# Performance work log

Hardware: AMD Instinct MI355X
Metric: run time of the kernel (lower is better)

## Reference

```python
import jax, jax.numpy as jnp
import numpy as np

B, D_IN, D_LAT, K = 8192, 768, 12288, 64


def setup_inputs() -> dict:
    key = jax.random.key(0)
    k1, k2, k3 = jax.random.split(key, 3)
    x = jax.random.normal(k1, (B, D_IN), dtype=jnp.float32)
    # Kaiming-uniform-ish init scale (matches nn.Linear default magnitude)
    W_enc = jax.random.normal(k2, (D_IN, D_LAT), dtype=jnp.float32) * (1.0 / np.sqrt(D_IN))
    b_enc = jnp.zeros((D_LAT,), dtype=jnp.float32)
    W_dec = jax.random.normal(k3, (D_LAT, D_IN), dtype=jnp.float32) * (1.0 / np.sqrt(D_LAT))
    b_dec = jnp.zeros((D_IN,), dtype=jnp.float32)
    return {"x": x, "W_enc": W_enc, "b_enc": b_enc, "W_dec": W_dec, "b_dec": b_dec, "k_top": K}


def topk_activation(h, k):
    # keep top-k values per row, zero the rest (equivalent to zeros_like + scatter_)
    if k >= h.shape[1]:
        return h
    vals, idx = jax.lax.top_k(h, k)                  # [B, k]
    rows = jnp.arange(h.shape[0])[:, None]           # [B, 1]
    return jnp.zeros_like(h).at[rows, idx].set(vals)


def reference(x, W_enc, b_enc, W_dec, b_dec, k_top):
    h = x @ W_enc + b_enc                            # [B, D_LAT]
    z = topk_activation(h, k_top)                    # sparse latent [B, D_LAT]
    recon = z @ W_dec + b_dec                        # [B, D_IN]
    return recon, z
```

## Files before the change

kernel.cpp:

```cpp
#include <hip/hip_runtime.h>
#include <stdint.h>

#define BROWS 8192
#define DIN   768
#define DLAT  12288
#define KTOP  64

#define LO_SCALE 4096.0f
#define LO_INV   (1.0f / 4096.0f)


typedef _Float16 half8 __attribute__((ext_vector_type(8)));
typedef __attribute__((ext_vector_type(4))) float float4v;

typedef __attribute__((address_space(3))) void lds_void_t;
typedef __attribute__((address_space(1))) void glob_void_t;

__device__ __forceinline__ unsigned short f2h_bits(float f) {
  _Float16 h = (_Float16)f;
  return __builtin_bit_cast(unsigned short, h);
}
__device__ __forceinline__ float h_bits_to_f(unsigned short b) {
  return (float)__builtin_bit_cast(_Float16, b);
}

__global__ __launch_bounds__(256) void k_cvt_split(const float* __restrict__ in,
                                                   unsigned short* __restrict__ hi,
                                                   unsigned short* __restrict__ lo,
                                                   int n4) {
  int i = blockIdx.x * 256 + threadIdx.x;
  if (i >= n4) return;
  float4 v = ((const float4*)in)[i];
  ushort4 h, l;
  h.x = f2h_bits(v.x); l.x = f2h_bits((v.x - h_bits_to_f(h.x)) * LO_SCALE);
  h.y = f2h_bits(v.y); l.y = f2h_bits((v.y - h_bits_to_f(h.y)) * LO_SCALE);
  h.z = f2h_bits(v.z); l.z = f2h_bits((v.z - h_bits_to_f(h.z)) * LO_SCALE);
  h.w = f2h_bits(v.w); l.w = f2h_bits((v.w - h_bits_to_f(h.w)) * LO_SCALE);
  ((ushort4*)hi)[i] = h;
  ((ushort4*)lo)[i] = l;
}

__global__ __launch_bounds__(256) void k_transpose_split(const float* __restrict__ W,
                                                         unsigned short* __restrict__ Wth,
                                                         unsigned short* __restrict__ Wtl) {
  __shared__ float s[32][33];
  const int n0 = blockIdx.x * 32;
  const int k0 = blockIdx.y * 32;
  const int tx = threadIdx.x, ty = threadIdx.y;
#pragma unroll
  for (int i = 0; i < 4; i++)
    s[ty + 8 * i][tx] = W[(size_t)(k0 + ty + 8 * i) * DLAT + n0 + tx];
  __syncthreads();
#pragma unroll
  for (int i = 0; i < 4; i++) {
    int nl = ty + 8 * i;
    float v = s[tx][nl];
    unsigned short h = f2h_bits(v);
    unsigned short l = f2h_bits((v - h_bits_to_f(h)) * LO_SCALE);
    size_t o = (size_t)(n0 + nl) * DIN + k0 + tx;
    Wth[o] = h;
    Wtl[o] = l;
  }
}

#define GBM 256
#define GBN 128
#define GBK 32

#define MFMA12(MI, AH, AL)                                                                   \
  do {                                                                                       \
    _Pragma("unroll") for (int ni = 0; ni < 4; ni++) {                                       \
      acc1[MI][ni] = __builtin_amdgcn_mfma_f32_16x16x32_f16(AH, bh[ni], acc1[MI][ni], 0, 0, 0); \
      acc2[MI][ni] = __builtin_amdgcn_mfma_f32_16x16x32_f16(AL, bh[ni], acc2[MI][ni], 0, 0, 0); \
      acc2[MI][ni] = __builtin_amdgcn_mfma_f32_16x16x32_f16(AH, bl[ni], acc2[MI][ni], 0, 0, 0); \
    }                                                                                        \
  } while (0)

#define STAGE1(R)                                                                            \
  __builtin_amdgcn_global_load_lds((glob_void_t*)(src[R] + kk2),                             \
                                   (lds_void_t*)(sb + loff[R]), 16, 0, 0)

__global__ __launch_bounds__(512, 2) void k_enc_gemm(const unsigned short* __restrict__ Xh,
                                                     const unsigned short* __restrict__ Xl,
                                                     const unsigned short* __restrict__ Wth,
                                                     const unsigned short* __restrict__ Wtl,
                                                     const float* __restrict__ b_enc,
                                                     float* __restrict__ H) {
  __shared__ unsigned short lds[3][24576];

  const int tid  = threadIdx.x;
  const int lane = tid & 63;
  const int wave = tid >> 6;
  const int wm   = wave >> 1;
  const int wn   = wave & 1;

  const int wg = (blockIdx.x & 7) * 384 + (blockIdx.x >> 3);
  const int tm = wg / 96;
  const int tn = wg - tm * 96;
  const int m_blk = tm * GBM;
  const int n_blk = tn * GBN;

  const int qlog = (lane & 3) ^ ((lane >> 3) & 3);
  const unsigned short* src[6];
  int loff[6];
#pragma unroll
  for (int r = 0; r < 6; r++) {
    const int c = wave * 6 + r;
    const unsigned short* base;
    int grow;
    if (c < 16)      { base = Xh;  grow = m_blk + c * 16; }
    else if (c < 32) { base = Xl;  grow = m_blk + (c - 16) * 16; }
    else if (c < 40) { base = Wth; grow = n_blk + (c - 32) * 16; }
    else             { base = Wtl; grow = n_blk + (c - 40) * 16; }
    src[r]  = base + (size_t)(grow + (lane >> 2)) * DIN + qlog * 8;
    loff[r] = c * 512;
  }

  const int qp   = (lane >> 4) ^ ((lane >> 1) & 3);
  const int aoff = (wm * 64 + (lane & 15)) * 32 + qp * 8;
  const int boff = 16384 + (wn * 64 + (lane & 15)) * 32 + qp * 8;

  float4v acc1[4][4];
  float4v acc2[4][4];
#pragma unroll
  for (int i = 0; i < 4; i++)
#pragma unroll
    for (int j = 0; j < 4; j++) { acc1[i][j] = (float4v)0.0f; acc2[i][j] = (float4v)0.0f; }

#pragma unroll
  for (int r = 0; r < 6; r++)
    __builtin_amdgcn_global_load_lds((glob_void_t*)(src[r]),
                                     (lds_void_t*)(&lds[0][loff[r]]), 16, 0, 0);
#pragma unroll
  for (int r = 0; r < 6; r++)
    __builtin_amdgcn_global_load_lds((glob_void_t*)(src[r] + GBK),
                                     (lds_void_t*)(&lds[1][loff[r]]), 16, 0, 0);
  asm volatile("s_waitcnt vmcnt(6)" ::: "memory");
  asm volatile("s_barrier" ::: "memory");

  const unsigned short* p_cur = lds[0];
  const unsigned short* p_nxt = lds[1];
  unsigned short*       p_stg = lds[2];

#pragma unroll 1
  for (int t = 0; t < 24; t++) {
    const unsigned short* lb = p_cur;
    unsigned short*       sb = p_stg;
    const int kk2 = t * GBK + 2 * GBK;
    const bool do_stage = (t < 22);

    half8 bh[4], bl[4], ah0, al0, ah1, al1;

#pragma unroll
    for (int ni = 0; ni < 4; ni++) {
      bh[ni] = *(const half8*)(lb + boff + ni * 512);
      bl[ni] = *(const half8*)(lb + boff + 4096 + ni * 512);
    }
    ah0 = *(const half8*)(lb + aoff);
    al0 = *(const half8*)(lb + aoff + 8192);
    ah1 = *(const half8*)(lb + aoff + 512);
    al1 = *(const half8*)(lb + aoff + 8192 + 512);
    if (do_stage) { STAGE1(0); STAGE1(1); STAGE1(2); }
    __builtin_amdgcn_s_setprio(1);
    MFMA12(0, ah0, al0);
    MFMA12(1, ah1, al1);
    __builtin_amdgcn_s_setprio(0);

    ah0 = *(const half8*)(lb + aoff + 1024);
    al0 = *(const half8*)(lb + aoff + 8192 + 1024);
    ah1 = *(const half8*)(lb + aoff + 1536);
    al1 = *(const half8*)(lb + aoff + 8192 + 1536);
    if (do_stage) { STAGE1(3); STAGE1(4); STAGE1(5); }
    __builtin_amdgcn_s_setprio(1);
    MFMA12(2, ah0, al0);
    MFMA12(3, ah1, al1);
    __builtin_amdgcn_s_setprio(0);

    asm volatile("s_waitcnt lgkmcnt(0)" ::: "memory");
    if (t < 22)       { asm volatile("s_waitcnt vmcnt(6)" ::: "memory"); }
    else if (t == 22) { asm volatile("s_waitcnt vmcnt(0)" ::: "memory"); }
    asm volatile("s_barrier" ::: "memory");

    const unsigned short* tmp = p_cur;
    p_cur = p_nxt;
    p_nxt = p_stg;
    p_stg = (unsigned short*)tmp;
  }

  const int col   = lane & 15;
  const int rbase = (lane >> 4) * 4;
#pragma unroll
  for (int ni = 0; ni < 4; ni++) {
    const int n = n_blk + wn * 64 + ni * 16 + col;
    const float bias = b_enc[n];
#pragma unroll
    for (int mi = 0; mi < 4; mi++) {
#pragma unroll
      for (int r = 0; r < 4; r++) {
        const int m = m_blk + wm * 64 + mi * 16 + rbase + r;
        H[(size_t)m * DLAT + n] = acc1[mi][ni][r] + acc2[mi][ni][r] * LO_INV + bias;
      }
    }
  }
}

#define UMARGIN 4e-4f
#define UCAP 64
__device__ __forceinline__ float key_to_f32(unsigned k) {
  unsigned u = (k & 0x80000000u) ? (k & 0x7fffffffu) : ~k;
  return __uint_as_float(u);
}
#define KIDX(J) (4 * tid + 1024 * ((J) >> 2) + ((J) & 3))

__global__ __launch_bounds__(256) void k_topk(float* __restrict__ Z,
                                              const float* __restrict__ x,
                                              const float* __restrict__ We,
                                              const float* __restrict__ b_enc,
                                              int* __restrict__ idxl,
                                              float* __restrict__ vall) {
  const int row = blockIdx.x;
  const int tid = threadIdx.x;
  const int lane = tid & 63, wid = tid >> 6;
  float* zr = Z + (size_t)row * DLAT;

  unsigned keys[48];
#pragma unroll
  for (int j4 = 0; j4 < 12; j4++) {
    const float4 v4 = ((const float4*)zr)[tid + 256 * j4];
    const float vv[4] = {v4.x, v4.y, v4.z, v4.w};
#pragma unroll
    for (int c = 0; c < 4; c++) {
      const unsigned u = __float_as_uint(vv[c]);
      keys[4 * j4 + c] = (u & 0x80000000u) ? ~u : (u | 0x80000000u);
    }
  }

  __shared__ int hist[1024];
  __shared__ unsigned s_cur;
  __shared__ int s_krem;
  __shared__ int s_nu, s_ncert, s_out;
  __shared__ int   u_idx[UCAP];
  __shared__ float u_vf[UCAP];
  __shared__ unsigned char u_sel[UCAP];

  if (tid == 0) { s_cur = 0u; s_krem = KTOP; }
  __syncthreads();

#pragma unroll
  for (int r = 0; r < 4; r++) {
    const int sh = 24 - 8 * r;
    const unsigned pre = s_cur;
    hist[tid] = 0; hist[tid + 256] = 0; hist[tid + 512] = 0; hist[tid + 768] = 0;
    __syncthreads();
#pragma unroll
    for (int j = 0; j < 48; j++) {
      const unsigned k = keys[j];
      if ((((unsigned long long)(k ^ pre)) >> (sh + 8)) == 0ull)
        atomicAdd(&hist[wid * 256 + ((k >> sh) & 255)], 1);
    }
    __syncthreads();
    if (wid == 0) {
      const int b0 = 4 * lane;
      int t0 = hist[b0]     + hist[256 + b0]     + hist[512 + b0]     + hist[768 + b0];
      int t1 = hist[b0 + 1] + hist[256 + b0 + 1] + hist[512 + b0 + 1] + hist[768 + b0 + 1];
      int t2 = hist[b0 + 2] + hist[256 + b0 + 2] + hist[512 + b0 + 2] + hist[768 + b0 + 2];
      int t3 = hist[b0 + 3] + hist[256 + b0 + 3] + hist[512 + b0 + 3] + hist[768 + b0 + 3];
      const int s3 = t3, s2 = t2 + s3, s1 = t1 + s2, s0 = t0 + s1;
      int hi = s0;
#pragma unroll
      for (int off = 1; off < 64; off <<= 1) {
        const int tmp = __shfl_down(hi, off);
        if (lane + off < 64) hi += tmp;
      }
      const int krem = s_krem;
      const int S0 = hi, S1 = hi - s0 + s1, S2 = hi - s0 + s2, S3 = hi - s0 + s3;
      int b = -1;
      if (S0 >= krem) b = b0;
      if (S1 >= krem) b = b0 + 1;
      if (S2 >= krem) b = b0 + 2;
      if (S3 >= krem) b = b0 + 3;
#pragma unroll
      for (int off = 1; off < 64; off <<= 1) b = max(b, __shfl_xor(b, off));
      if ((b >> 2) == lane) {
        const int c = b & 3;
        const int Sb = (c == 0) ? S0 : (c == 1) ? S1 : (c == 2) ? S2 : S3;
        const int tc = (c == 0) ? t0 : (c == 1) ? t1 : (c == 2) ? t2 : t3;
        s_krem = krem - (Sb - tc);
        s_cur  = pre | ((unsigned)b << sh);
      }
    }
    __syncthreads();
  }
  const unsigned cur = s_cur;
  const float h64 = key_to_f32(cur);

  if (tid == 0) { s_nu = 0; s_ncert = 0; s_out = 0; }
  __syncthreads();

  signed char uslot[48];
  int certc = 0;
#pragma unroll
  for (int j = 0; j < 48; j++) {
    const float v = key_to_f32(keys[j]);
    uslot[j] = -1;
    if (v > h64 + UMARGIN) {
      certc++;
    } else if (v >= h64 - UMARGIN) {
      int pos = atomicAdd(&s_nu, 1);
      if (pos < UCAP) {
        u_idx[pos] = KIDX(j);
        u_vf[pos]  = v;
        uslot[j] = (signed char)pos;
      }
    }
  }
  if (certc) atomicAdd(&s_ncert, certc);
  __syncthreads();

  const int nu = min(s_nu, UCAP);
  int t = KTOP - s_ncert;
  t = max(0, min(t, nu));

  if (nu > t) {
    if (tid < nu) {
      const int ci = u_idx[tid];
      const float* xr = x + (size_t)row * DIN;
      float c = 0.0f;
      for (int k = 0; k < DIN; k++)
        c = fmaf(xr[k], We[(size_t)k * DLAT + ci], c);
      u_vf[tid] = c + b_enc[ci];
    }
    __syncthreads();
    if (tid == 0) {
      for (int u = 0; u < nu; u++) {
        int rank = 0;
        for (int v2 = 0; v2 < nu; v2++)
          rank += (u_vf[v2] > u_vf[u]) ||
                  (u_vf[v2] == u_vf[u] && u_idx[v2] > u_idx[u]);
        u_sel[u] = (rank < t) ? 1 : 0;
      }
    }
  } else {
    if (tid < nu) u_sel[tid] = 1;
  }
  __syncthreads();

#pragma unroll
  for (int j4 = 0; j4 < 12; j4++) {
    float oc[4];
#pragma unroll
    for (int c = 0; c < 4; c++) {
      const int j = 4 * j4 + c;
      const int idx = 4 * tid + 1024 * j4 + c;
      const float v = key_to_f32(keys[j]);
      bool sel = false;
      float outv = 0.0f;
      if (v > h64 + UMARGIN) {
        sel = true; outv = v;
      } else if (uslot[j] >= 0 && u_sel[(int)uslot[j]]) {
        sel = true; outv = u_vf[(int)uslot[j]];
      }
      oc[c] = sel ? outv : 0.0f;
      if (sel) {
        int s = atomicAdd(&s_out, 1);
        if (s < KTOP) {
          idxl[row * KTOP + s] = idx;
          vall[row * KTOP + s] = outv;
        }
      }
    }
    float4 o;
    o.x = oc[0]; o.y = oc[1]; o.z = oc[2]; o.w = oc[3];
    ((float4*)zr)[tid + 256 * j4] = o;
  }
}

__global__ __launch_bounds__(192) void k_dec(const int* __restrict__ idxl,
                                             const float* __restrict__ vall,
                                             const float* __restrict__ Wd,
                                             const float* __restrict__ b_dec,
                                             float* __restrict__ R) {
  const int row = blockIdx.x;
  const int t = threadIdx.x;
  __shared__ int   sidx[KTOP];
  __shared__ float sval[KTOP];
  if (t < KTOP) {
    sidx[t] = idxl[row * KTOP + t];
    sval[t] = vall[row * KTOP + t];
  }
  __syncthreads();
  const int c = t * 4;
  float4 acc = *(const float4*)(b_dec + c);
#pragma unroll 4
  for (int j = 0; j < KTOP; j++) {
    float4 w = *(const float4*)(Wd + (size_t)sidx[j] * DIN + c);
    const float v = sval[j];
    acc.x += v * w.x;
    acc.y += v * w.y;
    acc.z += v * w.z;
    acc.w += v * w.w;
  }
  *(float4*)(R + (size_t)row * DIN + c) = acc;
}

extern "C" void kernel_launch(void* const* d_in, const int* in_sizes, int n_in,
                              void* d_out, int out_size, void* d_ws, size_t ws_size,
                              hipStream_t stream) {
  const float* x     = (const float*)d_in[0];
  const float* W_enc = (const float*)d_in[1];
  const float* b_enc = (const float*)d_in[2];
  const float* W_dec = (const float*)d_in[3];
  const float* b_dec = (const float*)d_in[4];

  float* recon = (float*)d_out;
  float* z     = (float*)d_out + (size_t)BROWS * DIN;

  unsigned short* Xh = (unsigned short*)recon;
  unsigned short* Xl = Xh + (size_t)BROWS * DIN;

  char* ws = (char*)d_ws;
  unsigned short* Wth = (unsigned short*)ws;
  unsigned short* Wtl = (unsigned short*)(ws + 18874368);
  int*   idxl = (int*)(ws + 2 * 18874368);
  float* vall = (float*)(ws + 2 * 18874368 + 2097152);

  k_cvt_split<<<6144, 256, 0, stream>>>(x, Xh, Xl, (BROWS * DIN) / 4);
  k_transpose_split<<<dim3(DLAT / 32, DIN / 32), dim3(32, 8), 0, stream>>>(W_enc, Wth, Wtl);
  k_enc_gemm<<<dim3(3072), dim3(512), 0, stream>>>(Xh, Xl, Wth, Wtl, b_enc, z);
  k_topk<<<BROWS, 256, 0, stream>>>(z, x, W_enc, b_enc, idxl, vall);
  k_dec<<<BROWS, 192, 0, stream>>>(idxl, vall, W_dec, b_dec, recon);
}
```

Before: 1.468 ms.

## Software-pipeline LDS fragment loads across k-iterations in the encoder GEMM

```diff
diff --git a/kernel.cpp b/kernel.cpp
--- a/kernel.cpp
+++ b/kernel.cpp
@@ -67,14 +67,16 @@
 #define GBN 128
 #define GBK 32
 
-#define MFMA12(MI, AH, AL)                                                                   \
-  do {                                                                                       \
-    _Pragma("unroll") for (int ni = 0; ni < 4; ni++) {                                       \
-      acc1[MI][ni] = __builtin_amdgcn_mfma_f32_16x16x32_f16(AH, bh[ni], acc1[MI][ni], 0, 0, 0); \
-      acc2[MI][ni] = __builtin_amdgcn_mfma_f32_16x16x32_f16(AL, bh[ni], acc2[MI][ni], 0, 0, 0); \
-      acc2[MI][ni] = __builtin_amdgcn_mfma_f32_16x16x32_f16(AH, bl[ni], acc2[MI][ni], 0, 0, 0); \
-    }                                                                                        \
-  } while (0)
+#define MFMA3(MI, NI, AH, AL, BH, BL)                                                        \
+  acc1[MI][NI] = __builtin_amdgcn_mfma_f32_16x16x32_f16(AH, BH, acc1[MI][NI], 0, 0, 0);      \
+  acc2[MI][NI] = __builtin_amdgcn_mfma_f32_16x16x32_f16(AL, BH, acc2[MI][NI], 0, 0, 0);      \
+  acc2[MI][NI] = __builtin_amdgcn_mfma_f32_16x16x32_f16(AH, BL, acc2[MI][NI], 0, 0, 0);
+
+#define CLUSTER(MI, AH, AL)                                                                  \
+  MFMA3(MI, 0, AH, AL, bh0, bl0)                                                             \
+  MFMA3(MI, 1, AH, AL, bh1, bl1)                                                             \
+  MFMA3(MI, 2, AH, AL, bh2, bl2)                                                             \
+  MFMA3(MI, 3, AH, AL, bh3, bl3)
 
 #define STAGE1(R)                                                                            \
   __builtin_amdgcn_global_load_lds((glob_void_t*)(src[R] + kk2),                             \
@@ -142,44 +144,65 @@
   const unsigned short* p_nxt = lds[1];
   unsigned short*       p_stg = lds[2];
 
+  half8 bh0 = *(const half8*)(p_cur + boff);
+  half8 bl0 = *(const half8*)(p_cur + boff + 4096);
+  half8 bh1 = *(const half8*)(p_cur + boff + 512);
+  half8 bl1 = *(const half8*)(p_cur + boff + 4096 + 512);
+  half8 bh2 = *(const half8*)(p_cur + boff + 1024);
+  half8 bl2 = *(const half8*)(p_cur + boff + 4096 + 1024);
+  half8 bh3 = *(const half8*)(p_cur + boff + 1536);
+  half8 bl3 = *(const half8*)(p_cur + boff + 4096 + 1536);
+  half8 pah0 = *(const half8*)(p_cur + aoff);
+  half8 pal0 = *(const half8*)(p_cur + aoff + 8192);
+  half8 pah1 = *(const half8*)(p_cur + aoff + 512);
+  half8 pal1 = *(const half8*)(p_cur + aoff + 8192 + 512);
+
 #pragma unroll 1
   for (int t = 0; t < 24; t++) {
     const unsigned short* lb = p_cur;
+    const unsigned short* nb = p_nxt;
     unsigned short*       sb = p_stg;
     const int kk2 = t * GBK + 2 * GBK;
-    const bool do_stage = (t < 22);
-
-    half8 bh[4], bl[4], ah0, al0, ah1, al1;
-
-#pragma unroll
-    for (int ni = 0; ni < 4; ni++) {
-      bh[ni] = *(const half8*)(lb + boff + ni * 512);
-      bl[ni] = *(const half8*)(lb + boff + 4096 + ni * 512);
-    }
-    ah0 = *(const half8*)(lb + aoff);
-    al0 = *(const half8*)(lb + aoff + 8192);
-    ah1 = *(const half8*)(lb + aoff + 512);
-    al1 = *(const half8*)(lb + aoff + 8192 + 512);
-    if (do_stage) { STAGE1(0); STAGE1(1); STAGE1(2); }
-    __builtin_amdgcn_s_setprio(1);
-    MFMA12(0, ah0, al0);
-    MFMA12(1, ah1, al1);
-    __builtin_amdgcn_s_setprio(0);
-
-    ah0 = *(const half8*)(lb + aoff + 1024);
-    al0 = *(const half8*)(lb + aoff + 8192 + 1024);
-    ah1 = *(const half8*)(lb + aoff + 1536);
-    al1 = *(const half8*)(lb + aoff + 8192 + 1536);
-    if (do_stage) { STAGE1(3); STAGE1(4); STAGE1(5); }
-    __builtin_amdgcn_s_setprio(1);
-    MFMA12(2, ah0, al0);
-    MFMA12(3, ah1, al1);
-    __builtin_amdgcn_s_setprio(0);
-
-    asm volatile("s_waitcnt lgkmcnt(0)" ::: "memory");
+
+    if (t < 22) { STAGE1(0); STAGE1(1); STAGE1(2); STAGE1(3); STAGE1(4); STAGE1(5); }
     if (t < 22)       { asm volatile("s_waitcnt vmcnt(6)" ::: "memory"); }
     else if (t == 22) { asm volatile("s_waitcnt vmcnt(0)" ::: "memory"); }
     asm volatile("s_barrier" ::: "memory");
+
+    half8 ah2 = *(const half8*)(lb + aoff + 1024);
+    half8 al2 = *(const half8*)(lb + aoff + 8192 + 1024);
+    half8 ah3 = *(const half8*)(lb + aoff + 1536);
+    half8 al3 = *(const half8*)(lb + aoff + 8192 + 1536);
+
+    __builtin_amdgcn_s_setprio(1);
+    CLUSTER(0, pah0, pal0)
+    CLUSTER(1, pah1, pal1)
+    __builtin_amdgcn_s_setprio(0);
+
+    half8 nbh0 = *(const half8*)(nb + boff);
+    half8 nbl0 = *(const half8*)(nb + boff + 4096);
+    half8 nbh1 = *(const half8*)(nb + boff + 512);
+    half8 nbl1 = *(const half8*)(nb + boff + 4096 + 512);
+    half8 nbh2 = *(const half8*)(nb + boff + 1024);
+    half8 nbl2 = *(const half8*)(nb + boff + 4096 + 1024);
+    half8 nbh3 = *(const half8*)(nb + boff + 1536);
+    half8 nbl3 = *(const half8*)(nb + boff + 4096 + 1536);
+    half8 nah0 = *(const half8*)(nb + aoff);
+    half8 nal0 = *(const half8*)(nb + aoff + 8192);
+    half8 nah1 = *(const half8*)(nb + aoff + 512);
+    half8 nal1 = *(const half8*)(nb + aoff + 8192 + 512);
+
+    __builtin_amdgcn_s_setprio(1);
+    CLUSTER(2, ah2, al2)
+    CLUSTER(3, ah3, al3)
+    __builtin_amdgcn_s_setprio(0);
+
+    asm volatile("s_waitcnt lgkmcnt(0)" ::: "memory");
+    asm volatile("s_barrier" ::: "memory");
+
+    bh0 = nbh0; bl0 = nbl0; bh1 = nbh1; bl1 = nbl1;
+    bh2 = nbh2; bl2 = nbl2; bh3 = nbh3; bl3 = nbl3;
+    pah0 = nah0; pal0 = nal0; pah1 = nah1; pal1 = nal1;
 
     const unsigned short* tmp = p_cur;
     p_cur = p_nxt;
```

New measurement: 1.532 ms. 1.04x slower.
